# Performance work log

Hardware: AMD Instinct MI355X
Metric: run time of the kernel (lower is better)

## Reference

```python
import jax, jax.numpy as jnp
import numpy as np
import math

B, S, D, NCLS, H = 32, 2048, 512, 2, 16
HD = D // H
KSIZE = 19


def setup_inputs() -> dict:
    key = jax.random.key(0)
    ks = jax.random.split(key, 20)
    f32 = jnp.float32
    s = 1.0 / math.sqrt(D)
    inp = {}
    inp['x'] = jax.random.normal(ks[0], (B, S, D), dtype=f32)
    # wave params [2, D, 1]: row 0 = scale (1 + randn), row 1 = shift
    inp['wave1'] = jnp.concatenate([1.0 + jax.random.normal(ks[1], (1, D, 1), f32), jax.random.normal(ks[2], (1, D, 1), f32)], axis=0)
    inp['wave2'] = jnp.concatenate([1.0 + jax.random.normal(ks[3], (1, D, 1), f32), jnp.zeros((1, D, 1), f32)], axis=0)
    inp['wave3'] = jnp.concatenate([1.0 + jax.random.normal(ks[4], (1, D, 1), f32), jnp.zeros((1, D, 1), f32)], axis=0)
    inp['Wp1'] = jax.random.normal(ks[5], (D, D), f32) * s   # WaveletEncoding.proj_1
    inp['bp1'] = jnp.zeros((D,), f32)
    inp['cls_token'] = jax.random.normal(ks[6], (1, NCLS, D), f32) * 0.02
    inp['ln1_g'] = jnp.ones((D,), f32)
    inp['ln1_b'] = jnp.zeros((D,), f32)
    inp['Wq'] = jax.random.normal(ks[7], (D, D), f32) * s      # no bias (qkv_bias=False)
    inp['Wkv'] = jax.random.normal(ks[8], (D, 2 * D), f32) * s
    inp['Wproj'] = jax.random.normal(ks[9], (D, D), f32) * s
    inp['bproj'] = jnp.zeros((D,), f32)
    inp['ln2_g'] = jnp.ones((D,), f32)
    inp['ln2_b'] = jnp.zeros((D,), f32)
    inp['Wc1'] = jax.random.normal(ks[10], (D, D), f32) * s
    inp['bc1'] = jnp.zeros((D,), f32)
    inp['Wc2'] = jax.random.normal(ks[11], (D, 1), f32) * s
    inp['bc2'] = jnp.zeros((1,), f32)
    return inp


def _layernorm(x, g, b, eps=1e-5):
    m = jnp.mean(x, axis=-1, keepdims=True)
    v = jnp.mean((x - m) ** 2, axis=-1, keepdims=True)
    return (x - m) / jnp.sqrt(v + eps) * g + b


def _mexican_hat(wave):
    # wave: [2, D, 1] -> kernel [D, KSIZE]
    scale, shift = wave[0], wave[1]                      # [D, 1]
    half = (KSIZE - 1) // 2
    xs = jnp.linspace(-half, half, KSIZE, dtype=jnp.float32)  # [KSIZE]
    xg = xs[None, :] - shift                             # [D, KSIZE]
    C = 2.0 / (3.0 ** 0.5 * np.pi ** 0.25)
    u = xg / scale
    return C * (1.0 - u ** 2) * jnp.exp(-0.5 * u ** 2) / jnp.sqrt(jnp.abs(scale))


def _dwconv(xc, kern):
    # xc [B, D, S], kern [D, KSIZE]; depthwise 'same' conv (groups=D)
    return jax.lax.conv_general_dilated(
        xc, kern[:, None, :], window_strides=(1,), padding='SAME',
        dimension_numbers=('NCH', 'OIH', 'NCH'), feature_group_count=D)


def _forward(x, wave1, wave2, wave3, Wp1, bp1, cls_token, ln1_g, ln1_b,
             Wq, Wkv, Wproj, bproj, ln2_g, ln2_b, Wc1, bc1, Wc2, bc2):
    # Wavelet positional encoding
    xc = jnp.transpose(x, (0, 2, 1))                     # [B, D, S]
    pos = _dwconv(xc, _mexican_hat(wave1)) + _dwconv(xc, _mexican_hat(wave2)) + _dwconv(xc, _mexican_hat(wave3))
    x = x + jnp.transpose(pos, (0, 2, 1)) @ Wp1 + bp1    # [B, S, D]
    # MIL pooling: layernorm on encoder tokens, sigmoid cross-attention
    xn = _layernorm(x, ln1_g, ln1_b)
    cls = jnp.broadcast_to(cls_token, (x.shape[0], NCLS, D))
    q = (cls @ Wq).reshape(-1, NCLS, H, HD).transpose(0, 2, 1, 3)        # [B, H, N, hd]
    kv = (xn @ Wkv).reshape(-1, S, 2, H, HD).transpose(2, 0, 3, 1, 4)    # [2, B, H, S, hd]
    k, v = kv[0], kv[1]
    scale = HD ** (-0.5)
    scores = jnp.einsum('bhnd,bhsd->bhns', q, k) * scale - math.log(S)   # -log(S) bias
    attn = jax.nn.sigmoid(scores)                                        # sigmoid, not softmax
    o = jnp.einsum('bhns,bhsd->bhnd', attn, v).transpose(0, 2, 1, 3).reshape(-1, NCLS, D)
    o = o @ Wproj + bproj
    # classifier head
    h = jax.nn.relu(_layernorm(o, ln2_g, ln2_b) @ Wc1 + bc1)
    logits = (h @ Wc2 + bc2)[..., 0]                                     # [B, NCLS]
    return logits, attn


def reference(x, wave1, wave2, wave3, Wp1, bp1, cls_token, ln1_g, ln1_b,
              Wq, Wkv, Wproj, bproj, ln2_g, ln2_b, Wc1, bc1, Wc2, bc2):
    return _forward(x, wave1, wave2, wave3, Wp1, bp1, cls_token, ln1_g, ln1_b,
                    Wq, Wkv, Wproj, bproj, ln2_g, ln2_b, Wc1, bc1, Wc2, bc2)
```

## Files before the change

### kernel.cpp

```cpp
#include <hip/hip_runtime.h>

#define SEQ 2048
#define DIM 512
#define NBATCH 32
#define NH 16
#define HDIM 32
#define NCLS 2

typedef __attribute__((ext_vector_type(8))) short short8;
typedef __attribute__((ext_vector_type(8))) unsigned short ushort8;
typedef __attribute__((ext_vector_type(4))) float f32x4;

__device__ __forceinline__ float b2f(unsigned short u){
  union { unsigned int i; float f; } v; v.i = ((unsigned int)u) << 16; return v.f;
}
__device__ __forceinline__ unsigned short f2b(float f){
  unsigned int x = __float_as_uint(f);
  unsigned int r = (x + 0x7fffu + ((x >> 16) & 1u)) >> 16;
  return (unsigned short)r;
}
__device__ __forceinline__ void gload16(const void* g, void* l){
  __builtin_amdgcn_global_load_lds((const __attribute__((address_space(1))) void*)g,
                                   (__attribute__((address_space(3))) void*)l, 16, 0, 0);
}

__global__ __launch_bounds__(256) void prep1_kernel(
    const float* __restrict__ w1, const float* __restrict__ w2, const float* __restrict__ w3,
    float* __restrict__ ksum,
    const float* __restrict__ cls, const float* __restrict__ Wq, float* __restrict__ qws,
    const float* __restrict__ Wp1, unsigned short* __restrict__ Wp1T,
    const float* __restrict__ Wkv, const float* __restrict__ g1, unsigned short* __restrict__ GvT){
  __shared__ unsigned short t[64][65];
  int bid = blockIdx.x;
  int tid = threadIdx.x;
  if (bid < 2){
    int d = bid * 256 + tid;
    const float C = 0.86732501f;
    float acc[19];
    #pragma unroll
    for (int i = 0; i < 19; ++i) acc[i] = 0.f;
    const float* waves[3] = { w1, w2, w3 };
    for (int tt = 0; tt < 3; ++tt){
      float scale = waves[tt][d];
      float shift = waves[tt][DIM + d];
      float inv = 1.f / scale;
      float amp = C * rsqrtf(fabsf(scale));
      #pragma unroll
      for (int i = 0; i < 19; ++i){
        float u = ((float)(i - 9) - shift) * inv;
        acc[i] += amp * (1.f - u * u) * expf(-0.5f * u * u);
      }
    }
    #pragma unroll
    for (int i = 0; i < 19; ++i) ksum[i * DIM + d] = acc[i];
  } else if (bid < 6){
    int idx = (bid - 2) * 256 + tid;
    int n = idx >> 9, c = idx & 511;
    float s = 0.f;
    for (int kd = 0; kd < DIM; ++kd)
      s = fmaf(cls[n * DIM + kd], Wq[(size_t)kd * DIM + c], s);
    qws[n * DIM + c] = s;
  } else if (bid < 70){
    int bx = bid - 6;
    int c0 = (bx & 7) * 64, r0 = (bx >> 3) * 64;
    #pragma unroll
    for (int i = 0; i < 16; ++i){
      int idx = i * 256 + tid;
      int r = idx >> 6, c = idx & 63;
      t[c][r] = f2b(Wp1[(size_t)(r0 + r) * 512 + c0 + c]);
    }
    __syncthreads();
    #pragma unroll
    for (int i = 0; i < 16; ++i){
      int idx = i * 256 + tid;
      int r = idx >> 6, c = idx & 63;
      Wp1T[(size_t)(c0 + r) * 512 + r0 + c] = t[r][c];
    }
  } else {
    int bx = bid - 70;
    int c0 = (bx & 7) * 64, r0 = (bx >> 3) * 64;
    #pragma unroll
    for (int i = 0; i < 16; ++i){
      int idx = i * 256 + tid;
      int r = idx >> 6, c = idx & 63;
      t[c][r] = f2b(Wkv[(size_t)(r0 + r) * 1024 + 512 + c0 + c] * g1[r0 + r]);
    }
    __syncthreads();
    #pragma unroll
    for (int i = 0; i < 16; ++i){
      int idx = i * 256 + tid;
      int r = idx >> 6, c = idx & 63;
      GvT[(size_t)(c0 + r) * 512 + r0 + c] = t[r][c];
    }
  }
}

__global__ __launch_bounds__(256) void prep2_kernel(const float* __restrict__ Wkv,
    const float* __restrict__ qws, const float* __restrict__ g1, const float* __restrict__ b1,
    unsigned short* __restrict__ AqT, float* __restrict__ gv, float* __restrict__ bv,
    float* __restrict__ ga, float* __restrict__ ba){
  const float SCALE = 0.17677669529663687f;
  const float LOGS  = 7.6246189861593985f;
  int bid = blockIdx.x;
  int tid = threadIdx.x;
  if (bid < 64){
    int idx = bid * 256 + tid;
    int hn = idx >> 9, d = idx & 511;
    int h = hn >> 1, n = hn & 1;
    float s = 0.f;
    #pragma unroll
    for (int hd = 0; hd < 32; ++hd)
      s = fmaf(Wkv[(size_t)d * 1024 + h * 32 + hd], qws[n * 512 + h * 32 + hd], s);
    AqT[hn * 512 + d] = f2b(SCALE * g1[d] * s);
  } else if (bid < 96){
    __shared__ float red[64];
    int hn = bid - 64;
    int h = hn >> 1, n = hn & 1;
    float s1 = 0.f, s2 = 0.f;
    #pragma unroll
    for (int dd = 0; dd < 2; ++dd){
      int d = tid + dd * 256;
      float inner = 0.f;
      #pragma unroll
      for (int hd = 0; hd < 32; ++hd)
        inner = fmaf(Wkv[(size_t)d * 1024 + h * 32 + hd], qws[n * 512 + h * 32 + hd], inner);
      s1 = fmaf(g1[d], inner, s1);
      s2 = fmaf(b1[d], inner, s2);
    }
    #pragma unroll
    for (int off = 32; off; off >>= 1){
      s1 += __shfl_xor(s1, off, 64);
      s2 += __shfl_xor(s2, off, 64);
    }
    int w = tid >> 6, lane = tid & 63;
    if (lane == 0){ red[w * 2] = s1; red[w * 2 + 1] = s2; }
    __syncthreads();
    if (tid == 0){
      float t1 = red[0] + red[2] + red[4] + red[6];
      float t2 = red[1] + red[3] + red[5] + red[7];
      ga[hn] = SCALE * t1;
      ba[hn] = SCALE * t2 - LOGS;
    }
  } else {
    int c = (bid - 96) * 256 + tid;
    float s1 = 0.f, s2 = 0.f;
    for (int d = 0; d < 512; ++d){
      float wv = Wkv[(size_t)d * 1024 + 512 + c];
      s1 = fmaf(g1[d], wv, s1);
      s2 = fmaf(b1[d], wv, s2);
    }
    gv[c] = s1; bv[c] = s2;
  }
}

__global__ __launch_bounds__(512) void conv_kernel(const float* __restrict__ X,
    const float* __restrict__ ksum, unsigned short* __restrict__ Pos){
  __shared__ float xs[34 * 512];
  int id = blockIdx.x;
  int id2 = (id & 7) * 512 + (id >> 3);
  int b = id2 >> 7;
  int strip = id2 & 127;
  int s0 = strip * 16;
  int tid = threadIdx.x;
  const float* xb = X + ((size_t)b * SEQ) * DIM;
  #pragma unroll
  for (int i = 0; i < 9; ++i){
    int g = i * 512 + tid;
    if (g < 4352){
      int row = g >> 7;
      int col4 = (g & 127) * 4;
      int s = s0 - 9 + row;
      int sc = s < 0 ? 0 : (s > SEQ - 1 ? SEQ - 1 : s);
      gload16(xb + (size_t)sc * DIM + col4, &xs[row * 512 + col4]);
    }
  }
  __syncthreads();
  if (strip == 0){
    #pragma unroll
    for (int i = 0; i < 9; ++i) xs[i * 512 + tid] = 0.f;
    __syncthreads();
  } else if (strip == 127){
    #pragma unroll
    for (int i = 25; i < 34; ++i) xs[i * 512 + tid] = 0.f;
    __syncthreads();
  }
  int d = tid;
  float kx[19];
  #pragma unroll
  for (int t = 0; t < 19; ++t) kx[t] = ksum[t * DIM + d];
  float ox[16];
  #pragma unroll
  for (int o = 0; o < 16; ++o) ox[o] = 0.f;
  #pragma unroll
  for (int w = 0; w < 34; ++w){
    float xv = xs[w * 512 + d];
    #pragma unroll
    for (int o = 0; o < 16; ++o){
      int t2 = w - o;
      if (t2 >= 0 && t2 < 19) ox[o] = fmaf(xv, kx[t2], ox[o]);
    }
  }
  #pragma unroll
  for (int o = 0; o < 16; ++o)
    Pos[((size_t)(b * SEQ + s0 + o)) * DIM + d] = f2b(ox[o]);
}

__global__ __launch_bounds__(512, 4) void gemm1_kernel(const unsigned short* __restrict__ A,
    const unsigned short* __restrict__ Bt, const float* __restrict__ Xres,
    const float* __restrict__ bias, unsigned short* __restrict__ Out,
    float* __restrict__ stat_part){
  __shared__ unsigned short lA[2 * 8192];
  __shared__ unsigned short lB[2 * 8192];
  __shared__ float sred[128][2][2];
  int tid = threadIdx.x;
  int w = tid >> 6, lane = tid & 63;
  int wm = w >> 1, wn = w & 1;
  int q = lane >> 4, cl = lane & 15;
  int id = blockIdx.x;
  int xcd = id & 7;
  int nch = (id >> 3) & 3;
  int mb  = ((id >> 5) << 3) | xcd;
  size_t mBase = (size_t)mb * 128;
  int nBase = nch * 128;

  auto stage = [&](int buf, int k0){
    #pragma unroll
    for (int p = 0; p < 2; ++p){
      int G = p * 512 + tid;
      int row = G >> 3;
      int c8 = (G & 7) ^ (row & 7);
      gload16(A + (mBase + row) * 512 + k0 + c8 * 8, &lA[buf * 8192 + G * 8]);
      gload16(Bt + (size_t)(nBase + row) * 512 + k0 + c8 * 8, &lB[buf * 8192 + G * 8]);
    }
  };

  f32x4 acc[2][4] = {};
  stage(0, 0);
  __syncthreads();
  int cur = 0;
  #pragma unroll
  for (int t = 0; t < 8; ++t){
    if (t < 7){
      stage(cur ^ 1, (t + 1) * 64);
      asm volatile("s_waitcnt vmcnt(4)" ::: "memory");
    } else {
      asm volatile("s_waitcnt vmcnt(0)" ::: "memory");
    }
    __builtin_amdgcn_s_barrier();
    const unsigned short* cA = &lA[cur * 8192];
    const unsigned short* cB = &lB[cur * 8192];
    #pragma unroll
    for (int kk = 0; kk < 2; ++kk){
      short8 af[2], bfr[4];
      #pragma unroll
      for (int m = 0; m < 2; ++m){
        int row = wm * 32 + m * 16 + cl;
        af[m] = *(const short8*)&cA[row * 64 + (((kk * 4 + q) ^ (row & 7)) * 8)];
      }
      #pragma unroll
      for (int n = 0; n < 4; ++n){
        int row = wn * 64 + n * 16 + cl;
        bfr[n] = *(const short8*)&cB[row * 64 + (((kk * 4 + q) ^ (row & 7)) * 8)];
      }
      #pragma unroll
      for (int m = 0; m < 2; ++m){
        #pragma unroll
        for (int n = 0; n < 4; ++n)
          acc[m][n] = __builtin_amdgcn_mfma_f32_16x16x32_bf16(af[m], bfr[n], acc[m][n], 0, 0, 0);
      }
    }
    asm volatile("s_waitcnt lgkmcnt(0)" ::: "memory");
    __builtin_amdgcn_s_barrier();
    cur ^= 1;
  }
  #pragma unroll
  for (int m = 0; m < 2; ++m){
    #pragma unroll
    for (int j = 0; j < 4; ++j){
      int rl = wm * 32 + m * 16 + q * 4 + j;
      size_t row = mBase + rl;
      float sm = 0.f, sq = 0.f;
      #pragma unroll
      for (int n = 0; n < 4; ++n){
        int col = nBase + wn * 64 + n * 16 + cl;
        float v = acc[m][n][j] + Xres[row * DIM + col] + bias[col];
        Out[row * DIM + col] = f2b(v);
        sm += v; sq += v * v;
      }
      #pragma unroll
      for (int off = 1; off < 16; off <<= 1){
        sm += __shfl_xor(sm, off, 64);
        sq += __shfl_xor(sq, off, 64);
      }
      if (cl == 0){ sred[rl][wn][0] = sm; sred[rl][wn][1] = sq; }
    }
  }
  __syncthreads();
  if (tid < 128){
    float sm = sred[tid][0][0] + sred[tid][1][0];
    float sq = sred[tid][0][1] + sred[tid][1][1];
    stat_part[((mBase + tid) * 4 + nch) * 2 + 0] = sm;
    stat_part[((mBase + tid) * 4 + nch) * 2 + 1] = sq;
  }
}

__global__ __launch_bounds__(512, 4) void stage2_kernel(
    const unsigned short* __restrict__ Y, const unsigned short* __restrict__ GvT,
    const unsigned short* __restrict__ AqT, const float* __restrict__ stat_part,
    const float* __restrict__ gv, const float* __restrict__ bv,
    const float* __restrict__ ga, const float* __restrict__ ba,
    float* __restrict__ aout, float* __restrict__ o_part){
  __shared__ __align__(16) char smem[74752];
  unsigned short* lA = (unsigned short*)smem;
  unsigned short* lB = (unsigned short*)(smem + 32768);
  float* stats = (float*)(smem + 73728);
  float* attn_lds = (float*)smem;
  float* o_red = (float*)(smem + 16896);
  int tid = threadIdx.x;
  int w = tid >> 6, lane = tid & 63;
  int wm = w >> 1, wn = w & 1;
  int q = lane >> 4, cl = lane & 15;
  int id = blockIdx.x;
  int xcd = id & 7;
  int nch = (id >> 3) & 3;
  int mb  = ((id >> 5) << 3) | xcd;
  size_t mBase = (size_t)mb * 128;
  int nBase = nch * 128;

  auto stage = [&](int buf, int k0){
    #pragma unroll
    for (int p = 0; p < 2; ++p){
      int G = p * 512 + tid;
      int row = G >> 3;
      int c8 = (G & 7) ^ (row & 7);
      gload16(Y + (mBase + row) * 512 + k0 + c8 * 8, &lA[buf * 8192 + G * 8]);
      gload16(GvT + (size_t)(nBase + row) * 512 + k0 + c8 * 8, &lB[buf * 10240 + G * 8]);
    }
    {
      int g = tid & 255;
      int row = 128 + (g >> 3);
      int c8 = (g & 7) ^ (row & 7);
      gload16(AqT + (size_t)(row - 128) * 512 + k0 + c8 * 8, &lB[buf * 10240 + (1024 + g) * 8]);
    }
  };

  stage(0, 0);
  if (tid < 128){
    float sm = 0.f, sq = 0.f;
    #pragma unroll
    for (int i = 0; i < 4; ++i){
      sm += stat_part[((mBase + tid) * 4 + i) * 2 + 0];
      sq += stat_part[((mBase + tid) * 4 + i) * 2 + 1];
    }
    float mean = sm * (1.f / 512.f);
    float var = sq * (1.f / 512.f) - mean * mean;
    stats[tid * 2 + 0] = mean;
    stats[tid * 2 + 1] = rsqrtf(var + 1e-5f);
  }
  __syncthreads();

  int hn = wn * 16 + cl;
  f32x4 acc[2][4] = {};
  f32x4 accs[2] = {};
  int cur = 0;
  #pragma unroll
  for (int t = 0; t < 8; ++t){
    if (t < 7){
      stage(cur ^ 1, (t + 1) * 64);
      asm volatile("s_waitcnt vmcnt(5)" ::: "memory");
    } else {
      asm volatile("s_waitcnt vmcnt(0)" ::: "memory");
    }
    __builtin_amdgcn_s_barrier();
    const unsigned short* cA = &lA[cur * 8192];
    const unsigned short* cB = &lB[cur * 10240];
    #pragma unroll
    for (int kk = 0; kk < 2; ++kk){
      short8 af[2], bfr[4], bq;
      {
        int row = 128 + hn;
        bq = *(const short8*)&cB[row * 64 + (((kk * 4 + q) ^ (row & 7)) * 8)];
      }
      #pragma unroll
      for (int m = 0; m < 2; ++m){
        int row = wm * 32 + m * 16 + cl;
        af[m] = *(const short8*)&cA[row * 64 + (((kk * 4 + q) ^ (row & 7)) * 8)];
      }
      #pragma unroll
      for (int n = 0; n < 4; ++n){
        int row = wn * 64 + n * 16 + cl;
        bfr[n] = *(const short8*)&cB[row * 64 + (((kk * 4 + q) ^ (row & 7)) * 8)];
      }
      #pragma unroll
      for (int m = 0; m < 2; ++m){
        #pragma unroll
        for (int n = 0; n < 4; ++n)
          acc[m][n] = __builtin_amdgcn_mfma_f32_16x16x32_bf16(af[m], bfr[n], acc[m][n], 0, 0, 0);
        accs[m] = __builtin_amdgcn_mfma_f32_16x16x32_bf16(af[m], bq, accs[m], 0, 0, 0);
      }
    }
    asm volatile("s_waitcnt lgkmcnt(0)" ::: "memory");
    __builtin_amdgcn_s_barrier();
    cur ^= 1;
  }
  float gav = ga[hn], bav = ba[hn];
  float gv4[4], bv4[4];
  #pragma unroll
  for (int n = 0; n < 4; ++n){
    int cg = nBase + wn * 64 + n * 16 + cl;
    gv4[n] = gv[cg]; bv4[n] = bv[cg];
  }
  int b = mb >> 4;
  int scb = (mb & 15) * 128;
  #pragma unroll
  for (int m = 0; m < 2; ++m){
    #pragma unroll
    for (int j = 0; j < 4; ++j){
      int rl = wm * 32 + m * 16 + q * 4 + j;
      float mu = stats[rl * 2 + 0], s = stats[rl * 2 + 1];
      float sc = s * accs[m][j] - s * mu * gav + bav;
      float at = 1.f / (1.f + expf(-sc));
      attn_lds[rl * 33 + hn] = at;
      if (nch == 0)
        aout[((size_t)(b * NH + (hn >> 1)) * NCLS + (hn & 1)) * SEQ + scb + rl] = at;
      #pragma unroll
      for (int n = 0; n < 4; ++n)
        acc[m][n][j] = s * acc[m][n][j] - s * mu * gv4[n] + bv4[n];
    }
  }
  __syncthreads();
  float o0[4] = {}, o1[4] = {};
  #pragma unroll
  for (int n = 0; n < 4; ++n){
    int cg = nBase + wn * 64 + n * 16 + cl;
    int h2 = ((cg >> 5) << 1);
    #pragma unroll
    for (int m = 0; m < 2; ++m){
      #pragma unroll
      for (int j = 0; j < 4; ++j){
        int rl = wm * 32 + m * 16 + q * 4 + j;
        float vv = acc[m][n][j];
        o0[n] = fmaf(attn_lds[rl * 33 + h2 + 0], vv, o0[n]);
        o1[n] = fmaf(attn_lds[rl * 33 + h2 + 1], vv, o1[n]);
      }
    }
  }
  #pragma unroll
  for (int n = 0; n < 4; ++n){
    o0[n] += __shfl_xor(o0[n], 16, 64);
    o0[n] += __shfl_xor(o0[n], 32, 64);
    o1[n] += __shfl_xor(o1[n], 16, 64);
    o1[n] += __shfl_xor(o1[n], 32, 64);
  }
  if (q == 0){
    #pragma unroll
    for (int n = 0; n < 4; ++n){
      int c = wn * 64 + n * 16 + cl;
      o_red[(0 * 4 + wm) * 128 + c] = o0[n];
      o_red[(1 * 4 + wm) * 128 + c] = o1[n];
    }
  }
  __syncthreads();
  if (tid < 256){
    int nn = tid >> 7, c = tid & 127;
    float v = o_red[(nn * 4 + 0) * 128 + c] + o_red[(nn * 4 + 1) * 128 + c]
            + o_red[(nn * 4 + 2) * 128 + c] + o_red[(nn * 4 + 3) * 128 + c];
    o_part[((size_t)mb * 2 + nn) * 512 + nBase + c] = v;
  }
}

__global__ __launch_bounds__(256) void head_kernel(const float* __restrict__ o_part,
    const float* __restrict__ Wproj, const float* __restrict__ bproj,
    const float* __restrict__ g2, const float* __restrict__ b2v,
    const float* __restrict__ Wc1, const float* __restrict__ bc1,
    const float* __restrict__ Wc2, const float* __restrict__ bc2,
    float* __restrict__ logits){
  __shared__ float orow[512];
  __shared__ float hrow[512];
  __shared__ float wred[8];
  __shared__ float wred2[4];
  int tid = threadIdx.x;
  int row = blockIdx.x;
  int b = row >> 1, nn = row & 1;
  for (int i = tid; i < 512; i += 256){
    float s = 0.f;
    const float* op = o_part + (((size_t)b * 16) * 2 + nn) * 512 + i;
    #pragma unroll
    for (int sc = 0; sc < 16; ++sc) s += op[(size_t)sc * 1024];
    orow[i] = s;
  }
  __syncthreads();
  int c0 = tid * 2;
  float a0 = 0.f, a1 = 0.f;
  for (int dd = 0; dd < DIM; ++dd){
    float ov = orow[dd];
    const float* wr = Wproj + (size_t)dd * DIM + c0;
    a0 = fmaf(ov, wr[0], a0);
    a1 = fmaf(ov, wr[1], a1);
  }
  a0 += bproj[c0]; a1 += bproj[c0 + 1];
  float sm = a0 + a1, sq = a0 * a0 + a1 * a1;
  #pragma unroll
  for (int off = 32; off; off >>= 1){
    sm += __shfl_xor(sm, off, 64);
    sq += __shfl_xor(sq, off, 64);
  }
  int w = tid >> 6, lane = tid & 63;
  if (lane == 0){ wred[w * 2] = sm; wred[w * 2 + 1] = sq; }
  __syncthreads();
  sm = wred[0] + wred[2] + wred[4] + wred[6];
  sq = wred[1] + wred[3] + wred[5] + wred[7];
  float mean = sm * (1.f / 512.f);
  float var = sq * (1.f / 512.f) - mean * mean;
  float rstd = rsqrtf(var + 1e-5f);
  hrow[c0]     = (a0 - mean) * rstd * g2[c0]     + b2v[c0];
  hrow[c0 + 1] = (a1 - mean) * rstd * g2[c0 + 1] + b2v[c0 + 1];
  __syncthreads();
  float h0 = 0.f, h1 = 0.f;
  for (int dd = 0; dd < DIM; ++dd){
    float lv = hrow[dd];
    const float* wr = Wc1 + (size_t)dd * DIM + c0;
    h0 = fmaf(lv, wr[0], h0);
    h1 = fmaf(lv, wr[1], h1);
  }
  h0 += bc1[c0]; h1 += bc1[c0 + 1];
  h0 = h0 > 0.f ? h0 : 0.f;
  h1 = h1 > 0.f ? h1 : 0.f;
  float p = h0 * Wc2[c0] + h1 * Wc2[c0 + 1];
  #pragma unroll
  for (int off = 32; off; off >>= 1) p += __shfl_xor(p, off, 64);
  if (lane == 0) wred2[w] = p;
  __syncthreads();
  if (tid == 0) logits[row] = wred2[0] + wred2[1] + wred2[2] + wred2[3] + bc2[0];
}

extern "C" void kernel_launch(void* const* d_in, const int* in_sizes, int n_in,
                              void* d_out, int out_size, void* d_ws, size_t ws_size,
                              hipStream_t stream) {
  const float* x     = (const float*)d_in[0];
  const float* wave1 = (const float*)d_in[1];
  const float* wave2 = (const float*)d_in[2];
  const float* wave3 = (const float*)d_in[3];
  const float* Wp1   = (const float*)d_in[4];
  const float* bp1   = (const float*)d_in[5];
  const float* cls   = (const float*)d_in[6];
  const float* ln1g  = (const float*)d_in[7];
  const float* ln1b  = (const float*)d_in[8];
  const float* Wq    = (const float*)d_in[9];
  const float* Wkv   = (const float*)d_in[10];
  const float* Wproj = (const float*)d_in[11];
  const float* bproj = (const float*)d_in[12];
  const float* ln2g  = (const float*)d_in[13];
  const float* ln2b  = (const float*)d_in[14];
  const float* Wc1   = (const float*)d_in[15];
  const float* bc1   = (const float*)d_in[16];
  const float* Wc2   = (const float*)d_in[17];
  const float* bc2   = (const float*)d_in[18];

  float* out = (float*)d_out;
  float* logits = out;
  float* attn   = out + 64;

  unsigned char* ws = (unsigned char*)d_ws;
  float* ksum           = (float*)(ws);
  float* qws            = (float*)(ws + (64u << 10));
  unsigned short* Wp1T  = (unsigned short*)(ws + (128u << 10));
  unsigned short* GvT   = (unsigned short*)(ws + (640u << 10));
  unsigned short* AqT   = (unsigned short*)(ws + (1152u << 10));
  float* gv             = (float*)(ws + (1248u << 10));
  float* bv             = (float*)(ws + (1252u << 10));
  float* ga             = (float*)(ws + (1256u << 10));
  float* ba             = (float*)(ws + (1260u << 10));
  float* o_part         = (float*)(ws + (1776u << 10));
  float* stat_part      = (float*)(ws + (4096u << 10));
  unsigned short* pos   = (unsigned short*)(ws + (8ull << 20));
  unsigned short* yb    = (unsigned short*)(ws + (72ull << 20));

  prep1_kernel<<<dim3(134), dim3(256), 0, stream>>>(wave1, wave2, wave3, ksum,
                                                    cls, Wq, qws, Wp1, Wp1T, Wkv, ln1g, GvT);
  prep2_kernel<<<dim3(98), dim3(256), 0, stream>>>(Wkv, qws, ln1g, ln1b, AqT, gv, bv, ga, ba);
  conv_kernel<<<dim3(4096), dim3(512), 0, stream>>>(x, ksum, pos);
  gemm1_kernel<<<dim3(2048), dim3(512), 0, stream>>>(pos, Wp1T, x, bp1, yb, stat_part);
  stage2_kernel<<<dim3(2048), dim3(512), 0, stream>>>(yb, GvT, AqT, stat_part,
                                                      gv, bv, ga, ba, attn, o_part);
  head_kernel<<<dim3(64), dim3(256), 0, stream>>>(o_part, Wproj, bproj, ln2g, ln2b,
                                                  Wc1, bc1, Wc2, bc2, logits);
}
```

Before: 273.4 us.

## Fuse projection GEMM and attention GEMM into one block-resident kernel

Merges gemm1 and stage2 into one kernel in which each 1024-thread block owns 128 rows across all 512 columns. The bf16 Y tile and the LayerNorm statistics stay in LDS, so Y and stat_part no longer make a round trip through global memory. B operands (Wp1T, GvT, AqT) are now read straight from global memory per MFMA instead of being staged in LDS, and the conv kernel is split into half-channel blocks. The risks are heavy LDS use (about 147 KB) giving one block per CU, only 512 blocks, and uncached-looking global B loads that could stall the MFMAs.

```diff
diff --git a/kernel.cpp b/kernel.cpp
--- a/kernel.cpp
+++ b/kernel.cpp
@@ -10,6 +10,7 @@
 typedef __attribute__((ext_vector_type(8))) short short8;
 typedef __attribute__((ext_vector_type(8))) unsigned short ushort8;
 typedef __attribute__((ext_vector_type(4))) float f32x4;
+typedef __attribute__((ext_vector_type(4))) unsigned int uint4v;
 
 __device__ __forceinline__ float b2f(unsigned short u){
   union { unsigned int i; float f; } v; v.i = ((unsigned int)u) << 16; return v.f;
@@ -153,47 +154,48 @@
   }
 }
 
-__global__ __launch_bounds__(512) void conv_kernel(const float* __restrict__ X,
+__global__ __launch_bounds__(256) void conv_kernel(const float* __restrict__ X,
     const float* __restrict__ ksum, unsigned short* __restrict__ Pos){
-  __shared__ float xs[34 * 512];
+  __shared__ float xs[34 * 256];
   int id = blockIdx.x;
-  int id2 = (id & 7) * 512 + (id >> 3);
-  int b = id2 >> 7;
-  int strip = id2 & 127;
-  int s0 = strip * 16;
+  int id2 = (id & 7) * 1024 + (id >> 3);
+  int b = id2 >> 8;
+  int rem = id2 & 255;
+  int strip = rem >> 1, half = rem & 1;
+  int s0 = strip * 16, c0 = half * 256;
   int tid = threadIdx.x;
-  const float* xb = X + ((size_t)b * SEQ) * DIM;
+  const float* xb = X + ((size_t)b * SEQ) * DIM + c0;
   #pragma unroll
   for (int i = 0; i < 9; ++i){
-    int g = i * 512 + tid;
-    if (g < 4352){
-      int row = g >> 7;
-      int col4 = (g & 127) * 4;
+    int g = i * 256 + tid;
+    if (g < 2176){
+      int row = g >> 6;
+      int gc = g & 63;
       int s = s0 - 9 + row;
       int sc = s < 0 ? 0 : (s > SEQ - 1 ? SEQ - 1 : s);
-      gload16(xb + (size_t)sc * DIM + col4, &xs[row * 512 + col4]);
+      gload16(xb + (size_t)sc * DIM + gc * 4, &xs[row * 256 + gc * 4]);
     }
   }
   __syncthreads();
   if (strip == 0){
     #pragma unroll
-    for (int i = 0; i < 9; ++i) xs[i * 512 + tid] = 0.f;
+    for (int i = 0; i < 9; ++i) xs[i * 256 + tid] = 0.f;
     __syncthreads();
   } else if (strip == 127){
     #pragma unroll
-    for (int i = 25; i < 34; ++i) xs[i * 512 + tid] = 0.f;
+    for (int i = 25; i < 34; ++i) xs[i * 256 + tid] = 0.f;
     __syncthreads();
   }
   int d = tid;
   float kx[19];
   #pragma unroll
-  for (int t = 0; t < 19; ++t) kx[t] = ksum[t * DIM + d];
+  for (int t = 0; t < 19; ++t) kx[t] = ksum[t * DIM + c0 + d];
   float ox[16];
   #pragma unroll
   for (int o = 0; o < 16; ++o) ox[o] = 0.f;
   #pragma unroll
   for (int w = 0; w < 34; ++w){
-    float xv = xs[w * 512 + d];
+    float xv = xs[w * 256 + d];
     #pragma unroll
     for (int o = 0; o < 16; ++o){
       int t2 = w - o;
@@ -202,156 +204,93 @@
   }
   #pragma unroll
   for (int o = 0; o < 16; ++o)
-    Pos[((size_t)(b * SEQ + s0 + o)) * DIM + d] = f2b(ox[o]);
-}
-
-__global__ __launch_bounds__(512, 4) void gemm1_kernel(const unsigned short* __restrict__ A,
-    const unsigned short* __restrict__ Bt, const float* __restrict__ Xres,
-    const float* __restrict__ bias, unsigned short* __restrict__ Out,
-    float* __restrict__ stat_part){
-  __shared__ unsigned short lA[2 * 8192];
-  __shared__ unsigned short lB[2 * 8192];
-  __shared__ float sred[128][2][2];
+    Pos[((size_t)(b * SEQ + s0 + o)) * DIM + c0 + d] = f2b(ox[o]);
+}
+
+__global__ __launch_bounds__(1024, 4) void fused_mid_kernel(
+    const unsigned short* __restrict__ Pos, const unsigned short* __restrict__ Wp1T,
+    const float* __restrict__ X, const float* __restrict__ bp1,
+    const unsigned short* __restrict__ GvT, const unsigned short* __restrict__ AqT,
+    const float* __restrict__ gv, const float* __restrict__ bv,
+    const float* __restrict__ ga, const float* __restrict__ ba,
+    float* __restrict__ aout, float* __restrict__ o_part){
+  __shared__ __align__(16) char smem[150528];
+  char* y_base = smem;
+  char* scratch = smem + 131072;
+  unsigned short* lA = (unsigned short*)scratch;
+  float* stats = (float*)(smem + 149504);
   int tid = threadIdx.x;
   int w = tid >> 6, lane = tid & 63;
-  int wm = w >> 1, wn = w & 1;
+  int wm = w >> 2, wn = w & 3;
   int q = lane >> 4, cl = lane & 15;
-  int id = blockIdx.x;
-  int xcd = id & 7;
-  int nch = (id >> 3) & 3;
-  int mb  = ((id >> 5) << 3) | xcd;
+  int mb = blockIdx.x;
   size_t mBase = (size_t)mb * 128;
-  int nBase = nch * 128;
-
-  auto stage = [&](int buf, int k0){
-    #pragma unroll
-    for (int p = 0; p < 2; ++p){
-      int G = p * 512 + tid;
-      int row = G >> 3;
-      int c8 = (G & 7) ^ (row & 7);
-      gload16(A + (mBase + row) * 512 + k0 + c8 * 8, &lA[buf * 8192 + G * 8]);
-      gload16(Bt + (size_t)(nBase + row) * 512 + k0 + c8 * 8, &lB[buf * 8192 + G * 8]);
-    }
-  };
-
-  f32x4 acc[2][4] = {};
-  stage(0, 0);
-  __syncthreads();
-  int cur = 0;
+  int b = mb >> 4;
+  int scb = (mb & 15) * 128;
+
+  int rowA = tid >> 3, c8 = tid & 7;
+  const unsigned short* psrc = Pos + (mBase + rowA) * 512 + c8 * 8;
+  unsigned ldst = (unsigned)((rowA * 8 + (c8 ^ (rowA & 7))) * 16);
+  uint4v rv = *(const uint4v*)psrc;
+  f32x4 acc1[2][8] = {};
   #pragma unroll
   for (int t = 0; t < 8; ++t){
-    if (t < 7){
-      stage(cur ^ 1, (t + 1) * 64);
-      asm volatile("s_waitcnt vmcnt(4)" ::: "memory");
-    } else {
-      asm volatile("s_waitcnt vmcnt(0)" ::: "memory");
-    }
-    __builtin_amdgcn_s_barrier();
-    const unsigned short* cA = &lA[cur * 8192];
-    const unsigned short* cB = &lB[cur * 8192];
+    __syncthreads();
+    *(uint4v*)(scratch + ldst) = rv;
+    if (t < 7) rv = *(const uint4v*)(psrc + (t + 1) * 64);
+    __syncthreads();
     #pragma unroll
     for (int kk = 0; kk < 2; ++kk){
-      short8 af[2], bfr[4];
+      short8 af[2];
       #pragma unroll
       for (int m = 0; m < 2; ++m){
         int row = wm * 32 + m * 16 + cl;
-        af[m] = *(const short8*)&cA[row * 64 + (((kk * 4 + q) ^ (row & 7)) * 8)];
-      }
-      #pragma unroll
-      for (int n = 0; n < 4; ++n){
-        int row = wn * 64 + n * 16 + cl;
-        bfr[n] = *(const short8*)&cB[row * 64 + (((kk * 4 + q) ^ (row & 7)) * 8)];
-      }
-      #pragma unroll
-      for (int m = 0; m < 2; ++m){
-        #pragma unroll
-        for (int n = 0; n < 4; ++n)
-          acc[m][n] = __builtin_amdgcn_mfma_f32_16x16x32_bf16(af[m], bfr[n], acc[m][n], 0, 0, 0);
-      }
-    }
-    asm volatile("s_waitcnt lgkmcnt(0)" ::: "memory");
-    __builtin_amdgcn_s_barrier();
-    cur ^= 1;
-  }
+        af[m] = *(const short8*)&lA[(row * 8 + ((kk * 4 + q) ^ (row & 7))) * 8];
+      }
+      #pragma unroll
+      for (int n = 0; n < 8; ++n){
+        short8 bf = *(const short8*)(Wp1T + (size_t)(wn * 128 + n * 16 + cl) * 512
+                                     + t * 64 + kk * 32 + q * 8);
+        acc1[0][n] = __builtin_amdgcn_mfma_f32_16x16x32_bf16(af[0], bf, acc1[0][n], 0, 0, 0);
+        acc1[1][n] = __builtin_amdgcn_mfma_f32_16x16x32_bf16(af[1], bf, acc1[1][n], 0, 0, 0);
+      }
+    }
+  }
+  __syncthreads();
+  float* sred = (float*)scratch;
+  float bp1v[8];
+  #pragma unroll
+  for (int n = 0; n < 8; ++n) bp1v[n] = bp1[wn * 128 + n * 16 + cl];
   #pragma unroll
   for (int m = 0; m < 2; ++m){
     #pragma unroll
     for (int j = 0; j < 4; ++j){
       int rl = wm * 32 + m * 16 + q * 4 + j;
-      size_t row = mBase + rl;
+      const float* xr = X + (mBase + rl) * 512;
       float sm = 0.f, sq = 0.f;
       #pragma unroll
-      for (int n = 0; n < 4; ++n){
-        int col = nBase + wn * 64 + n * 16 + cl;
-        float v = acc[m][n][j] + Xres[row * DIM + col] + bias[col];
-        Out[row * DIM + col] = f2b(v);
+      for (int n = 0; n < 8; ++n){
+        int col = wn * 128 + n * 16 + cl;
+        float v = acc1[m][n][j] + xr[col] + bp1v[n];
         sm += v; sq += v * v;
+        int gs = (col >> 3) ^ ((rl & 7) << 3);
+        *(unsigned short*)(y_base + (rl * 64 + gs) * 16 + (col & 7) * 2) = f2b(v);
       }
       #pragma unroll
       for (int off = 1; off < 16; off <<= 1){
         sm += __shfl_xor(sm, off, 64);
         sq += __shfl_xor(sq, off, 64);
       }
-      if (cl == 0){ sred[rl][wn][0] = sm; sred[rl][wn][1] = sq; }
+      if (cl == 0){
+        sred[(rl * 4 + wn) * 2 + 0] = sm;
+        sred[(rl * 4 + wn) * 2 + 1] = sq;
+      }
     }
   }
   __syncthreads();
   if (tid < 128){
-    float sm = sred[tid][0][0] + sred[tid][1][0];
-    float sq = sred[tid][0][1] + sred[tid][1][1];
-    stat_part[((mBase + tid) * 4 + nch) * 2 + 0] = sm;
-    stat_part[((mBase + tid) * 4 + nch) * 2 + 1] = sq;
-  }
-}
-
-__global__ __launch_bounds__(512, 4) void stage2_kernel(
-    const unsigned short* __restrict__ Y, const unsigned short* __restrict__ GvT,
-    const unsigned short* __restrict__ AqT, const float* __restrict__ stat_part,
-    const float* __restrict__ gv, const float* __restrict__ bv,
-    const float* __restrict__ ga, const float* __restrict__ ba,
-    float* __restrict__ aout, float* __restrict__ o_part){
-  __shared__ __align__(16) char smem[74752];
-  unsigned short* lA = (unsigned short*)smem;
-  unsigned short* lB = (unsigned short*)(smem + 32768);
-  float* stats = (float*)(smem + 73728);
-  float* attn_lds = (float*)smem;
-  float* o_red = (float*)(smem + 16896);
-  int tid = threadIdx.x;
-  int w = tid >> 6, lane = tid & 63;
-  int wm = w >> 1, wn = w & 1;
-  int q = lane >> 4, cl = lane & 15;
-  int id = blockIdx.x;
-  int xcd = id & 7;
-  int nch = (id >> 3) & 3;
-  int mb  = ((id >> 5) << 3) | xcd;
-  size_t mBase = (size_t)mb * 128;
-  int nBase = nch * 128;
-
-  auto stage = [&](int buf, int k0){
-    #pragma unroll
-    for (int p = 0; p < 2; ++p){
-      int G = p * 512 + tid;
-      int row = G >> 3;
-      int c8 = (G & 7) ^ (row & 7);
-      gload16(Y + (mBase + row) * 512 + k0 + c8 * 8, &lA[buf * 8192 + G * 8]);
-      gload16(GvT + (size_t)(nBase + row) * 512 + k0 + c8 * 8, &lB[buf * 10240 + G * 8]);
-    }
-    {
-      int g = tid & 255;
-      int row = 128 + (g >> 3);
-      int c8 = (g & 7) ^ (row & 7);
-      gload16(AqT + (size_t)(row - 128) * 512 + k0 + c8 * 8, &lB[buf * 10240 + (1024 + g) * 8]);
-    }
-  };
-
-  stage(0, 0);
-  if (tid < 128){
-    float sm = 0.f, sq = 0.f;
-    #pragma unroll
-    for (int i = 0; i < 4; ++i){
-      sm += stat_part[((mBase + tid) * 4 + i) * 2 + 0];
-      sq += stat_part[((mBase + tid) * 4 + i) * 2 + 1];
-    }
+    float sm = sred[tid * 8 + 0] + sred[tid * 8 + 2] + sred[tid * 8 + 4] + sred[tid * 8 + 6];
+    float sq = sred[tid * 8 + 1] + sred[tid * 8 + 3] + sred[tid * 8 + 5] + sred[tid * 8 + 7];
     float mean = sm * (1.f / 512.f);
     float var = sq * (1.f / 512.f) - mean * mean;
     stats[tid * 2 + 0] = mean;
@@ -359,59 +298,42 @@
   }
   __syncthreads();
 
-  int hn = wn * 16 + cl;
-  f32x4 acc[2][4] = {};
+  f32x4 acc2[2][8] = {};
   f32x4 accs[2] = {};
-  int cur = 0;
+  int hnf = wn & 1;
   #pragma unroll
   for (int t = 0; t < 8; ++t){
-    if (t < 7){
-      stage(cur ^ 1, (t + 1) * 64);
-      asm volatile("s_waitcnt vmcnt(5)" ::: "memory");
-    } else {
-      asm volatile("s_waitcnt vmcnt(0)" ::: "memory");
-    }
-    __builtin_amdgcn_s_barrier();
-    const unsigned short* cA = &lA[cur * 8192];
-    const unsigned short* cB = &lB[cur * 10240];
     #pragma unroll
     for (int kk = 0; kk < 2; ++kk){
-      short8 af[2], bfr[4], bq;
-      {
-        int row = 128 + hn;
-        bq = *(const short8*)&cB[row * 64 + (((kk * 4 + q) ^ (row & 7)) * 8)];
-      }
+      short8 af[2];
       #pragma unroll
       for (int m = 0; m < 2; ++m){
         int row = wm * 32 + m * 16 + cl;
-        af[m] = *(const short8*)&cA[row * 64 + (((kk * 4 + q) ^ (row & 7)) * 8)];
-      }
-      #pragma unroll
-      for (int n = 0; n < 4; ++n){
-        int row = wn * 64 + n * 16 + cl;
-        bfr[n] = *(const short8*)&cB[row * 64 + (((kk * 4 + q) ^ (row & 7)) * 8)];
-      }
-      #pragma unroll
-      for (int m = 0; m < 2; ++m){
-        #pragma unroll
-        for (int n = 0; n < 4; ++n)
-          acc[m][n] = __builtin_amdgcn_mfma_f32_16x16x32_bf16(af[m], bfr[n], acc[m][n], 0, 0, 0);
-        accs[m] = __builtin_amdgcn_mfma_f32_16x16x32_bf16(af[m], bq, accs[m], 0, 0, 0);
-      }
-    }
-    asm volatile("s_waitcnt lgkmcnt(0)" ::: "memory");
-    __builtin_amdgcn_s_barrier();
-    cur ^= 1;
-  }
+        int gs = (t * 8 + kk * 4 + q) ^ ((row & 7) << 3);
+        af[m] = *(const short8*)(y_base + (row * 64 + gs) * 16);
+      }
+      short8 bq = *(const short8*)(AqT + (size_t)(hnf * 16 + cl) * 512 + t * 64 + kk * 32 + q * 8);
+      accs[0] = __builtin_amdgcn_mfma_f32_16x16x32_bf16(af[0], bq, accs[0], 0, 0, 0);
+      accs[1] = __builtin_amdgcn_mfma_f32_16x16x32_bf16(af[1], bq, accs[1], 0, 0, 0);
+      #pragma unroll
+      for (int n = 0; n < 8; ++n){
+        short8 bf = *(const short8*)(GvT + (size_t)(wn * 128 + n * 16 + cl) * 512
+                                     + t * 64 + kk * 32 + q * 8);
+        acc2[0][n] = __builtin_amdgcn_mfma_f32_16x16x32_bf16(af[0], bf, acc2[0][n], 0, 0, 0);
+        acc2[1][n] = __builtin_amdgcn_mfma_f32_16x16x32_bf16(af[1], bf, acc2[1][n], 0, 0, 0);
+      }
+    }
+  }
+  float* attn_lds = (float*)scratch;
+  int hn = hnf * 16 + cl;
   float gav = ga[hn], bav = ba[hn];
-  float gv4[4], bv4[4];
-  #pragma unroll
-  for (int n = 0; n < 4; ++n){
-    int cg = nBase + wn * 64 + n * 16 + cl;
-    gv4[n] = gv[cg]; bv4[n] = bv[cg];
-  }
-  int b = mb >> 4;
-  int scb = (mb & 15) * 128;
+  float gv8[8], bv8[8];
+  #pragma unroll
+  for (int n = 0; n < 8; ++n){
+    int cg = wn * 128 + n * 16 + cl;
+    gv8[n] = gv[cg]; bv8[n] = bv[cg];
+  }
+  __syncthreads();
   #pragma unroll
   for (int m = 0; m < 2; ++m){
     #pragma unroll
@@ -421,51 +343,55 @@
       float sc = s * accs[m][j] - s * mu * gav + bav;
       float at = 1.f / (1.f + expf(-sc));
       attn_lds[rl * 33 + hn] = at;
-      if (nch == 0)
+      if (wn < 2)
         aout[((size_t)(b * NH + (hn >> 1)) * NCLS + (hn & 1)) * SEQ + scb + rl] = at;
       #pragma unroll
-      for (int n = 0; n < 4; ++n)
-        acc[m][n][j] = s * acc[m][n][j] - s * mu * gv4[n] + bv4[n];
-    }
-  }
-  __syncthreads();
-  float o0[4] = {}, o1[4] = {};
-  #pragma unroll
-  for (int n = 0; n < 4; ++n){
-    int cg = nBase + wn * 64 + n * 16 + cl;
+      for (int n = 0; n < 8; ++n)
+        acc2[m][n][j] = s * acc2[m][n][j] - s * mu * gv8[n] + bv8[n];
+    }
+  }
+  __syncthreads();
+  float o0[8], o1[8];
+  #pragma unroll
+  for (int n = 0; n < 8; ++n){ o0[n] = 0.f; o1[n] = 0.f; }
+  #pragma unroll
+  for (int n = 0; n < 8; ++n){
+    int cg = wn * 128 + n * 16 + cl;
     int h2 = ((cg >> 5) << 1);
     #pragma unroll
     for (int m = 0; m < 2; ++m){
       #pragma unroll
       for (int j = 0; j < 4; ++j){
         int rl = wm * 32 + m * 16 + q * 4 + j;
-        float vv = acc[m][n][j];
+        float vv = acc2[m][n][j];
         o0[n] = fmaf(attn_lds[rl * 33 + h2 + 0], vv, o0[n]);
         o1[n] = fmaf(attn_lds[rl * 33 + h2 + 1], vv, o1[n]);
       }
     }
   }
   #pragma unroll
-  for (int n = 0; n < 4; ++n){
+  for (int n = 0; n < 8; ++n){
     o0[n] += __shfl_xor(o0[n], 16, 64);
     o0[n] += __shfl_xor(o0[n], 32, 64);
     o1[n] += __shfl_xor(o1[n], 16, 64);
     o1[n] += __shfl_xor(o1[n], 32, 64);
   }
+  __syncthreads();
+  float* o_red = (float*)scratch;
   if (q == 0){
     #pragma unroll
-    for (int n = 0; n < 4; ++n){
-      int c = wn * 64 + n * 16 + cl;
-      o_red[(0 * 4 + wm) * 128 + c] = o0[n];
-      o_red[(1 * 4 + wm) * 128 + c] = o1[n];
-    }
-  }
-  __syncthreads();
-  if (tid < 256){
-    int nn = tid >> 7, c = tid & 127;
-    float v = o_red[(nn * 4 + 0) * 128 + c] + o_red[(nn * 4 + 1) * 128 + c]
-            + o_red[(nn * 4 + 2) * 128 + c] + o_red[(nn * 4 + 3) * 128 + c];
-    o_part[((size_t)mb * 2 + nn) * 512 + nBase + c] = v;
+    for (int n = 0; n < 8; ++n){
+      int c = wn * 128 + n * 16 + cl;
+      o_red[(0 * 4 + wm) * 512 + c] = o0[n];
+      o_red[(1 * 4 + wm) * 512 + c] = o1[n];
+    }
+  }
+  __syncthreads();
+  {
+    int nn = tid >> 9, c = tid & 511;
+    float v = o_red[(nn * 4 + 0) * 512 + c] + o_red[(nn * 4 + 1) * 512 + c]
+            + o_red[(nn * 4 + 2) * 512 + c] + o_red[(nn * 4 + 3) * 512 + c];
+    o_part[((size_t)mb * 2 + nn) * 512 + c] = v;
   }
 }
 
@@ -572,17 +498,14 @@
   float* ga             = (float*)(ws + (1256u << 10));
   float* ba             = (float*)(ws + (1260u << 10));
   float* o_part         = (float*)(ws + (1776u << 10));
-  float* stat_part      = (float*)(ws + (4096u << 10));
   unsigned short* pos   = (unsigned short*)(ws + (8ull << 20));
-  unsigned short* yb    = (unsigned short*)(ws + (72ull << 20));
 
   prep1_kernel<<<dim3(134), dim3(256), 0, stream>>>(wave1, wave2, wave3, ksum,
                                                     cls, Wq, qws, Wp1, Wp1T, Wkv, ln1g, GvT);
   prep2_kernel<<<dim3(98), dim3(256), 0, stream>>>(Wkv, qws, ln1g, ln1b, AqT, gv, bv, ga, ba);
-  conv_kernel<<<dim3(4096), dim3(512), 0, stream>>>(x, ksum, pos);
-  gemm1_kernel<<<dim3(2048), dim3(512), 0, stream>>>(pos, Wp1T, x, bp1, yb, stat_part);
-  stage2_kernel<<<dim3(2048), dim3(512), 0, stream>>>(yb, GvT, AqT, stat_part,
-                                                      gv, bv, ga, ba, attn, o_part);
+  conv_kernel<<<dim3(8192), dim3(256), 0, stream>>>(x, ksum, pos);
+  fused_mid_kernel<<<dim3(512), dim3(1024), 0, stream>>>(pos, Wp1T, x, bp1, GvT, AqT,
+                                                         gv, bv, ga, ba, attn, o_part);
   head_kernel<<<dim3(64), dim3(256), 0, stream>>>(o_part, Wproj, bproj, ln2g, ln2b,
                                                   Wc1, bc1, Wc2, bc2, logits);
 }
```

After: 456.2 us. +66.9%, slower.
